# Kernel tuning notes

Hardware: AMD Instinct MI355X
Metric: run time of the kernel (lower is better)

## Reference

```python
import jax, jax.numpy as jnp
import numpy as np

DT = 0.001  # euler step size (module default dt)
T = 2000    # num_timesteps
N_IN = 8192
N_OUT = 4096


def setup_inputs() -> dict:
    key = jax.random.key(0)
    k_x, k_w = jax.random.split(key)
    x = jax.random.normal(k_x, (T, N_IN), dtype=jnp.float32)
    # module initializes weight.data.uniform_(-0.1, 0.1)
    weight = jax.random.uniform(k_w, (N_OUT, N_IN), dtype=jnp.float32, minval=-0.1, maxval=0.1)
    ones = jnp.ones((N_OUT,), dtype=jnp.float32)
    # default_lif_parameters broadcast to per-neuron vectors (constant_lif_parameters)
    return {
        "x": x,
        "weight": weight,
        "v_th": ones * 75.0,
        "v_rest": ones * 50.0,
        "v_reset": ones * 30.0,
        "t_ref": ones * 0.001,
        "tau": ones * 2.0,
    }


def reference(x, weight, v_th, v_rest, v_reset, t_ref, tau):
    # lif_input[t] = x[t] @ weight.T  -> [T, N_OUT]
    lif_input = x @ weight.T

    def step(carry, inp):
        v, refrac = carry
        # leak toward v_rest
        v = v - DT * tau * (v - v_rest)
        # integrate input only when not refractory
        v = v + jnp.where(refrac == 0, inp, jnp.zeros_like(inp))
        # count down refractory period
        refrac = jnp.where(refrac > 0, refrac - DT, jnp.zeros_like(refrac))
        # heavyside spike
        spike = (v - v_th >= 0).astype(v.dtype)
        sb = spike > 0
        # reset: refractory period and membrane potential
        refrac = jnp.where(sb, t_ref, refrac)
        v = jnp.where(sb, v_reset, v)
        return (v, refrac), spike

    v0 = v_rest.astype(x.dtype)               # v[0] = v_rest
    refrac0 = jnp.zeros_like(v0)
    # torch loop runs i = 1 .. T-1 consuming lif_input[i]
    _, spikes = jax.lax.scan(step, (v0, refrac0), lif_input[1:])
    s0 = jnp.zeros((1, spikes.shape[1]), dtype=spikes.dtype)  # s[0] stays zero
    return jnp.concatenate([s0, spikes], axis=0)  # [T, N_OUT]
```

## Files before the change

### kernel.cpp

```cpp
#include <hip/hip_runtime.h>
#include <hip/hip_bf16.h>


#define T_STEPS 2000
#define NIN_K   8192
#define NOUT_N  4096
#define MPAD    2048

typedef __attribute__((ext_vector_type(8))) _Float16 half8;
typedef __attribute__((ext_vector_type(4))) float f32x4;

#define GLL16(g, l)                                                              \
    __builtin_amdgcn_global_load_lds(                                            \
        (const __attribute__((address_space(1))) void*)(g),                      \
        (__attribute__((address_space(3))) void*)(l), 16, 0, 0)

__global__ __launch_bounds__(256) void split_f32(const float* __restrict__ src,
                                                 _Float16* __restrict__ hi,
                                                 _Float16* __restrict__ lo,
                                                 size_t n_valid) {
    const size_t i8 = (size_t)(blockIdx.x * 256u + threadIdx.x) * 8;
    float vv[8];
    if (i8 < n_valid) {
        float4 v0 = *(const float4*)(src + i8);
        float4 v1 = *(const float4*)(src + i8 + 4);
        vv[0] = v0.x; vv[1] = v0.y; vv[2] = v0.z; vv[3] = v0.w;
        vv[4] = v1.x; vv[5] = v1.y; vv[6] = v1.z; vv[7] = v1.w;
    } else {
#pragma unroll
        for (int j = 0; j < 8; ++j) vv[j] = 0.f;
    }
    half8 h8, l8;
#pragma unroll
    for (int j = 0; j < 8; ++j) {
        _Float16 h = (_Float16)vv[j];
        float r = __fsub_rn(vv[j], (float)h);
        h8[j] = h;
        l8[j] = (_Float16)(r * 4096.0f);
    }
    *(half8*)(hi + i8) = h8;
    *(half8*)(lo + i8) = l8;
}

__global__ __launch_bounds__(256, 2) void gemm_f16x2(const _Float16* __restrict__ A0,
                                                     const _Float16* __restrict__ A1,
                                                     const _Float16* __restrict__ B0,
                                                     const _Float16* __restrict__ B1,
                                                     float* __restrict__ C) {
    __shared__ _Float16 lds[4][128 * 64];

    const int tid  = threadIdx.x;
    const int wave = tid >> 6;
    const int lane = tid & 63;
    const int bm = blockIdx.y * 128;
    const int bn = blockIdx.x * 128;
    const int wm = (wave >> 1) * 64;
    const int wn = (wave & 1) * 64;

    const int srow = tid >> 3;
    const int skswz = ((tid & 7) ^ (srow & 7)) * 8;

    f32x4 acc0[4][4], acc1[4][4];
#pragma unroll
    for (int i = 0; i < 4; ++i)
#pragma unroll
        for (int j = 0; j < 4; ++j) {
            acc0[i][j] = (f32x4){0.f, 0.f, 0.f, 0.f};
            acc1[i][j] = (f32x4){0.f, 0.f, 0.f, 0.f};
        }

    const int quad = lane >> 4;
    const int l16  = lane & 15;

    for (int k0 = 0; k0 < NIN_K; k0 += 64) {
        __syncthreads();
#pragma unroll
        for (int c = 0; c < 4; ++c) {
            const size_t ga = (size_t)(bm + c * 32 + srow) * NIN_K + k0 + skswz;
            const size_t gb = (size_t)(bn + c * 32 + srow) * NIN_K + k0 + skswz;
            const int base = (c * 32 + wave * 8) * 64;
            GLL16(A0 + ga, &lds[0][base]);
            GLL16(A1 + ga, &lds[1][base]);
            GLL16(B0 + gb, &lds[2][base]);
            GLL16(B1 + gb, &lds[3][base]);
        }
        __syncthreads();

#pragma unroll
        for (int ks = 0; ks < 2; ++ks) {
            half8 b0f[4], b1f[4];
#pragma unroll
            for (int j = 0; j < 4; ++j) {
                const int row = wn + j * 16 + l16;
                const int off = row * 64 + ((ks * 4 + quad) ^ (row & 7)) * 8;
                b0f[j] = *(const half8*)&lds[2][off];
                b1f[j] = *(const half8*)&lds[3][off];
            }
#pragma unroll
            for (int i = 0; i < 4; ++i) {
                const int row = wm + i * 16 + l16;
                const int off = row * 64 + ((ks * 4 + quad) ^ (row & 7)) * 8;
                const half8 a0f = *(const half8*)&lds[0][off];
                const half8 a1f = *(const half8*)&lds[1][off];
#pragma unroll
                for (int j = 0; j < 4; ++j) {
                    acc0[i][j] = __builtin_amdgcn_mfma_f32_16x16x32_f16(a0f, b0f[j], acc0[i][j], 0, 0, 0);
                    acc1[i][j] = __builtin_amdgcn_mfma_f32_16x16x32_f16(a0f, b1f[j], acc1[i][j], 0, 0, 0);
                    acc1[i][j] = __builtin_amdgcn_mfma_f32_16x16x32_f16(a1f, b0f[j], acc1[i][j], 0, 0, 0);
                }
            }
        }
    }

    const float s = 1.0f / 4096.0f;
#pragma unroll
    for (int i = 0; i < 4; ++i)
#pragma unroll
        for (int j = 0; j < 4; ++j) {
            const int m = bm + wm + i * 16 + quad * 4;
            const int n = bn + wn + j * 16 + l16;
            float* cp = C + (size_t)m * NOUT_N + n;
#pragma unroll
            for (int r = 0; r < 4; ++r)
                cp[(size_t)r * NOUT_N] = __fmaf_rn(acc1[i][j][r], s, acc0[i][j][r]);
        }
}

#define BM 64
#define BN 64
#define BK 16
#define PAD 4
__global__ __launch_bounds__(256) void gemm_bt(const float* __restrict__ A,
                                               const float* __restrict__ B,
                                               float* __restrict__ C,
                                               int M, int N, int K) {
    __shared__ float As[BK][BM + PAD];
    __shared__ float Bs[BK][BN + PAD];
    const int bm = blockIdx.y * BM, bn = blockIdx.x * BN;
    const int tid = threadIdx.x;
    const int tx = tid & 15, ty = tid >> 4;
    const int lrow = tid >> 2, lk = (tid & 3) * 4;
    float acc[4][4];
#pragma unroll
    for (int i = 0; i < 4; ++i)
#pragma unroll
        for (int j = 0; j < 4; ++j) acc[i][j] = 0.0f;
    for (int k0 = 0; k0 < K; k0 += BK) {
        const int am = bm + lrow;
        float4 av = (am < M) ? *(const float4*)(A + (size_t)am * K + k0 + lk)
                             : make_float4(0.f, 0.f, 0.f, 0.f);
        As[lk + 0][lrow] = av.x; As[lk + 1][lrow] = av.y;
        As[lk + 2][lrow] = av.z; As[lk + 3][lrow] = av.w;
        float4 bv = *(const float4*)(B + (size_t)(bn + lrow) * K + k0 + lk);
        Bs[lk + 0][lrow] = bv.x; Bs[lk + 1][lrow] = bv.y;
        Bs[lk + 2][lrow] = bv.z; Bs[lk + 3][lrow] = bv.w;
        __syncthreads();
#pragma unroll
        for (int k = 0; k < BK; ++k) {
            float a[4], b[4];
#pragma unroll
            for (int i = 0; i < 4; ++i) a[i] = As[k][ty * 4 + i];
#pragma unroll
            for (int j = 0; j < 4; ++j) b[j] = Bs[k][tx * 4 + j];
#pragma unroll
            for (int i = 0; i < 4; ++i)
#pragma unroll
                for (int j = 0; j < 4; ++j) acc[i][j] += a[i] * b[j];
        }
        __syncthreads();
    }
#pragma unroll
    for (int i = 0; i < 4; ++i) {
        const int m = bm + ty * 4 + i;
        if (m < M) {
            float* cp = C + (size_t)m * N + bn + tx * 4;
#pragma unroll
            for (int j = 0; j < 4; ++j) cp[j] = acc[i][j];
        }
    }
}

__global__ void zero_rows(float* __restrict__ p, size_t n) {
    const size_t i = (size_t)blockIdx.x * 256 + threadIdx.x;
    if (i < n) p[i] = 0.0f;
}

__global__ __launch_bounds__(64) void lif_scan(const float* __restrict__ inp,
                                               const float* __restrict__ v_th_p,
                                               const float* __restrict__ v_rest_p,
                                               const float* __restrict__ v_reset_p,
                                               const float* __restrict__ t_ref_p,
                                               const float* __restrict__ tau_p,
                                               float* __restrict__ out) {
    const int j = blockIdx.x * 64 + threadIdx.x;
    const int N = NOUT_N;
    const float vth = v_th_p[j], vrest = v_rest_p[j], vres = v_reset_p[j];
    const float tref = t_ref_p[j];
    const float c = __fmul_rn(0.001f, tau_p[j]);
    float v = vrest, refrac = 0.0f;
    out[j] = 0.0f;

    float pf[16];
#pragma unroll
    for (int d = 0; d < 16; ++d) pf[d] = inp[(size_t)(1 + d) * N + j];

    for (int g = 0; g < 124; ++g) {
        const int tbase = 1 + g * 16;
#pragma unroll
        for (int d = 0; d < 16; ++d) {
            const int t = tbase + d;
            const float in = pf[d];
            pf[d] = inp[(size_t)(t + 16) * N + j];
            const float dd = __fmul_rn(c, __fsub_rn(v, vrest));
            v = __fsub_rn(v, dd);
            v = (refrac == 0.0f) ? __fadd_rn(v, in) : v;
            refrac = (refrac > 0.0f) ? (refrac - 0.001f) : 0.0f;
            const bool s = (__fsub_rn(v, vth) >= 0.0f);
            out[(size_t)t * N + j] = s ? 1.0f : 0.0f;
            refrac = s ? tref : refrac;
            v = s ? vres : v;
        }
    }
#pragma unroll
    for (int e = 0; e < 15; ++e) {
        const int t = 1985 + e;
        const float in = pf[e];
        const float dd = __fmul_rn(c, __fsub_rn(v, vrest));
        v = __fsub_rn(v, dd);
        v = (refrac == 0.0f) ? __fadd_rn(v, in) : v;
        refrac = (refrac > 0.0f) ? (refrac - 0.001f) : 0.0f;
        const bool s = (__fsub_rn(v, vth) >= 0.0f);
        out[(size_t)t * N + j] = s ? 1.0f : 0.0f;
        refrac = s ? tref : refrac;
        v = s ? vres : v;
    }
}

extern "C" void kernel_launch(void* const* d_in, const int* in_sizes, int n_in,
                              void* d_out, int out_size, void* d_ws, size_t ws_size,
                              hipStream_t stream) {
    const float* x       = (const float*)d_in[0];
    const float* w       = (const float*)d_in[1];
    const float* v_th    = (const float*)d_in[2];
    const float* v_rest  = (const float*)d_in[3];
    const float* v_reset = (const float*)d_in[4];
    const float* t_ref   = (const float*)d_in[5];
    const float* tau     = (const float*)d_in[6];
    float* out = (float*)d_out;

    const size_t LIF_B = (size_t)MPAD * NOUT_N * 4;
    const size_t XS_B  = (size_t)MPAD * NIN_K * 2;
    const size_t WS_B  = (size_t)NOUT_N * NIN_K * 2;
    const size_t NEED  = LIF_B + 2 * XS_B + 2 * WS_B;

    char* ws = (char*)d_ws;
    float* lif = (float*)ws;

    if (ws_size >= NEED) {
        _Float16* x0 = (_Float16*)(ws + LIF_B);
        _Float16* x1 = (_Float16*)(ws + LIF_B + XS_B);
        _Float16* w0 = (_Float16*)(ws + LIF_B + 2 * XS_B);
        _Float16* w1 = (_Float16*)(ws + LIF_B + 2 * XS_B + WS_B);

        const size_t nx = (size_t)MPAD * NIN_K;
        split_f32<<<nx / 8 / 256, 256, 0, stream>>>(x, x0, x1,
                                                    (size_t)T_STEPS * NIN_K);
        const size_t nw = (size_t)NOUT_N * NIN_K;
        split_f32<<<nw / 8 / 256, 256, 0, stream>>>(w, w0, w1, nw);

        dim3 g(NOUT_N / 128, MPAD / 128);
        gemm_f16x2<<<g, 256, 0, stream>>>(x0, x1, w0, w1, lif);
    } else {
        dim3 g(NOUT_N / BN, (T_STEPS + BM - 1) / BM);
        gemm_bt<<<g, 256, 0, stream>>>(x, w, lif, T_STEPS, NOUT_N, NIN_K);
        const size_t padn = (size_t)(MPAD - T_STEPS) * NOUT_N;
        zero_rows<<<(padn + 255) / 256, 256, 0, stream>>>(lif + (size_t)T_STEPS * NOUT_N, padn);
    }

    lif_scan<<<NOUT_N / 64, 64, 0, stream>>>(lif, v_th, v_rest, v_reset, t_ref, tau, out);
}
```

Baseline: 721.9 us.

## Stream LIF scan inputs through an LDS ring via global_load_lds prefetch

Replaces the per-thread register prefetch of scan inputs in lif_scan with a 16-slot LDS ring buffer. The ring is filled with 16-byte global_load_lds transfers covering four timesteps per chunk, and each chunk's values are read into registers two chunks ahead. The aim is to hide global load latency on the serial recurrence and to use wider loads. The steady-state wait is vmcnt(63), and the output stores also count toward vmcnt, so the ring data may not be guaranteed to have landed before it is read.

```diff
diff --git a/kernel.cpp b/kernel.cpp
--- a/kernel.cpp
+++ b/kernel.cpp
@@ -192,48 +192,80 @@
                                                const float* __restrict__ t_ref_p,
                                                const float* __restrict__ tau_p,
                                                float* __restrict__ out) {
-    const int j = blockIdx.x * 64 + threadIdx.x;
+    __shared__ float ring[16 * 256];
+    const int lane  = threadIdx.x;
+    const int jbase = blockIdx.x * 64;
+    const int j = jbase + lane;
     const int N = NOUT_N;
+
     const float vth = v_th_p[j], vrest = v_rest_p[j], vres = v_reset_p[j];
     const float tref = t_ref_p[j];
-    const float c = __fmul_rn(0.001f, tau_p[j]);
+    const float cleak = __fmul_rn(0.001f, tau_p[j]);
     float v = vrest, refrac = 0.0f;
     out[j] = 0.0f;
 
-    float pf[16];
-#pragma unroll
-    for (int d = 0; d < 16; ++d) pf[d] = inp[(size_t)(1 + d) * N + j];
-
-    for (int g = 0; g < 124; ++g) {
-        const int tbase = 1 + g * 16;
-#pragma unroll
-        for (int d = 0; d < 16; ++d) {
-            const int t = tbase + d;
-            const float in = pf[d];
-            pf[d] = inp[(size_t)(t + 16) * N + j];
-            const float dd = __fmul_rn(c, __fsub_rn(v, vrest));
-            v = __fsub_rn(v, dd);
-            v = (refrac == 0.0f) ? __fadd_rn(v, in) : v;
-            refrac = (refrac > 0.0f) ? (refrac - 0.001f) : 0.0f;
-            const bool s = (__fsub_rn(v, vth) >= 0.0f);
-            out[(size_t)t * N + j] = s ? 1.0f : 0.0f;
-            refrac = s ? tref : refrac;
-            v = s ? vres : v;
-        }
-    }
-#pragma unroll
-    for (int e = 0; e < 15; ++e) {
-        const int t = 1985 + e;
-        const float in = pf[e];
-        const float dd = __fmul_rn(c, __fsub_rn(v, vrest));
-        v = __fsub_rn(v, dd);
-        v = (refrac == 0.0f) ? __fadd_rn(v, in) : v;
-        refrac = (refrac > 0.0f) ? (refrac - 0.001f) : 0.0f;
-        const bool s = (__fsub_rn(v, vth) >= 0.0f);
-        out[(size_t)t * N + j] = s ? 1.0f : 0.0f;
-        refrac = s ? tref : refrac;
-        v = s ? vres : v;
-    }
+    const int lrow = lane >> 4;
+    const int lcol = (lane & 15) * 4;
+
+#define GLLC(cx)                                                                  \
+    {                                                                             \
+        const float* _src = inp + (size_t)(4 * (cx) + lrow) * NOUT_N + jbase + lcol; \
+        GLL16(_src, &ring[((cx) & 15) * 256]);                                    \
+    }
+
+#define STEP(t, in)                                                               \
+    {                                                                             \
+        const float dd = __fmul_rn(cleak, __fsub_rn(v, vrest));                   \
+        v = __fsub_rn(v, dd);                                                     \
+        v = (refrac == 0.0f) ? __fadd_rn(v, (in)) : v;                            \
+        refrac = (refrac > 0.0f) ? (refrac - 0.001f) : 0.0f;                      \
+        const bool s = (__fsub_rn(v, vth) >= 0.0f);                               \
+        out[(size_t)(t) * N + j] = s ? 1.0f : 0.0f;                               \
+        refrac = s ? tref : refrac;                                               \
+        v = s ? vres : v;                                                         \
+    }
+
+#define HALF(cc, WAITSTR, P0, P1, P2, P3)                                         \
+    {                                                                             \
+        if ((cc) + 16 <= 511) GLLC((cc) + 16);                                    \
+        asm volatile(WAITSTR ::: "memory");                                       \
+        const int _slot = (((cc) + 2) & 15) * 256;                                \
+        const float _n0 = ring[_slot + 0 * 64 + lane];                            \
+        const float _n1 = ring[_slot + 1 * 64 + lane];                            \
+        const float _n2 = ring[_slot + 2 * 64 + lane];                            \
+        const float _n3 = ring[_slot + 3 * 64 + lane];                            \
+        const int _tb = 4 * (cc);                                                 \
+        if (_tb != 0) STEP(_tb, P0);                \
+        STEP(_tb + 1, P1);                                                        \
+        STEP(_tb + 2, P2);                                                        \
+        STEP(_tb + 3, P3);                                                        \
+        P0 = _n0; P1 = _n1; P2 = _n2; P3 = _n3;                                   \
+    }
+
+#pragma unroll
+    for (int c0 = 0; c0 < 16; ++c0) GLLC(c0);
+    asm volatile("s_waitcnt vmcnt(14)" ::: "memory");
+    float pa0 = ring[0 * 256 + 0 * 64 + lane];
+    float pa1 = ring[0 * 256 + 1 * 64 + lane];
+    float pa2 = ring[0 * 256 + 2 * 64 + lane];
+    float pa3 = ring[0 * 256 + 3 * 64 + lane];
+    float pb0 = ring[1 * 256 + 0 * 64 + lane];
+    float pb1 = ring[1 * 256 + 1 * 64 + lane];
+    float pb2 = ring[1 * 256 + 2 * 64 + lane];
+    float pb3 = ring[1 * 256 + 3 * 64 + lane];
+
+    for (int cc = 0; cc < 14; cc += 2) {
+        HALF(cc,     "s_waitcnt vmcnt(14)", pa0, pa1, pa2, pa3);
+        HALF(cc + 1, "s_waitcnt vmcnt(14)", pb0, pb1, pb2, pb3);
+    }
+    for (int cc = 14; cc < 500; cc += 2) {
+        HALF(cc,     "s_waitcnt vmcnt(63)", pa0, pa1, pa2, pa3);
+        HALF(cc + 1, "s_waitcnt vmcnt(63)", pb0, pb1, pb2, pb3);
+    }
+
+#undef HALF
+#undef STEP
+#undef GLLC
 }
 
 extern "C" void kernel_launch(void* const* d_in, const int* in_sizes, int n_in,
```

New measurement: 721.8 us. No clear change (-0.0%).
